# Optimization experiments

Hardware: AMD Instinct MI355X
Metric: run time of the kernel (lower is better)

The kernel has to match this reference:

```python
import jax, jax.numpy as jnp
import numpy as np

N_NODES = 50000
N_EDGES = 800000
D_IN = 64
D_OUT = 64


def setup_inputs() -> dict:
    key = jax.random.key(0)
    ks = jax.random.split(key, 7)
    features = jax.random.normal(ks[0], (N_NODES, D_IN), dtype=jnp.float32)
    # Linear(in,out,bias=False) weight: (out_features, in_features)
    W = jax.random.normal(ks[1], (D_OUT, D_IN), dtype=jnp.float32) / np.sqrt(D_IN)
    bias = jnp.zeros((D_OUT,), dtype=jnp.float32)
    skip_weight = jnp.ones((D_OUT,), dtype=jnp.float32)
    # sparse normalized adjacency as an edge list with scalar weights
    edge_src = jax.random.randint(ks[2], (N_EDGES,), 0, N_NODES, dtype=jnp.int32)
    edge_dst = jax.random.randint(ks[3], (N_EDGES,), 0, N_NODES, dtype=jnp.int32)
    edge_weight = jax.random.uniform(ks[4], (N_EDGES,), dtype=jnp.float32)
    return {
        "features": features,
        "W": W,
        "bias": bias,
        "skip_weight": skip_weight,
        "edge_weight": edge_weight,
        "edge_src": edge_src,
        "edge_dst": edge_dst,
    }


def reference(features, W, bias, skip_weight, edge_weight, edge_src, edge_dst):
    # Feature transform: x @ W^T  -> (n, out_features)
    h = jnp.einsum("nd,od->no", features, W)
    # Skip term: elementwise scale of transformed features
    skip = h * skip_weight
    # Sparse SpMM: aggregate weighted neighbor messages
    msgs = h[edge_src] * edge_weight[:, None]          # (E, out)
    agg = jax.ops.segment_sum(msgs, edge_dst, num_segments=N_NODES)  # (n, out)
    out = skip + agg + bias
    return jax.nn.selu(out)
```

## Files before the change

### kernel.cpp

```cpp
#include <hip/hip_runtime.h>
#include <math.h>

#define N_NODES 50000
#define N_EDGES 800000
#define D 64
#define NB2 782
#define BCAP2 2048
#define EPB 4096
#define NSCAT 196
#define GROWS 128
#define NGEMM ((N_NODES + GROWS - 1) / GROWS)

__device__ __forceinline__ float selu_f(float x) {
    const float scale = 1.0507009873554805f;
    const float alpha = 1.6732632423543772f;
    return x > 0.0f ? scale * x : scale * alpha * expm1f(x);
}

__device__ __forceinline__ unsigned int f2bf(float x) {
    unsigned int u = __float_as_uint(x);
    u += 0x7FFFu + ((u >> 16) & 1u);
    return u >> 16;
}

__device__ __forceinline__ float bf2f(unsigned int b) {
    return __uint_as_float(b << 16);
}

__global__ __launch_bounds__(1024) void fused_gemm_scatter(const float* __restrict__ feat,
                                                           const float* __restrict__ W,
                                                           const int* __restrict__ edst,
                                                           const int* __restrict__ esrc,
                                                           const float* __restrict__ ew,
                                                           unsigned short* __restrict__ hb,
                                                           int* __restrict__ gcursor,
                                                           int2* __restrict__ pay) {
    extern __shared__ char smem[];
    const int tid = threadIdx.x;

    if (blockIdx.x < NSCAT) {
        int* hist    = (int*)smem;
        int* lexcl   = hist + NB2;
        int* gbase   = lexcl + NB2;
        int* waveAgg = gbase + NB2;
        int2* stage  = (int2*)(waveAgg + 16);

        const int wid = tid >> 6;
        const int lane = tid & 63;
        const int e0 = blockIdx.x * EPB;
        const int cntb = min(EPB, N_EDGES - e0);

        for (int i = tid; i < NB2; i += 1024) hist[i] = 0;
        __syncthreads();

        int2 rec[4];
        int rb[4];
#pragma unroll
        for (int k = 0; k < 4; ++k) {
            const int idx = k * 1024 + tid;
            rb[k] = -1;
            if (idx < cntb) {
                const int e = e0 + idx;
                const int dst = edst[e];
                const int b = dst >> 6;
                rb[k] = b;
                rec[k] = make_int2((esrc[e] & 0xFFFF) | ((dst & 63) << 16) | (b << 22),
                                   __float_as_int(ew[e]));
                atomicAdd(&hist[b], 1);
            }
        }
        __syncthreads();

        const int v = (tid < NB2) ? hist[tid] : 0;
        int incl = v;
#pragma unroll
        for (int off = 1; off < 64; off <<= 1) {
            const int t = __shfl_up(incl, off);
            if (lane >= off) incl += t;
        }
        if (lane == 63) waveAgg[wid] = incl;
        __syncthreads();
        if (wid == 0) {
            const int wv = (lane < 16) ? waveAgg[lane] : 0;
            int wincl = wv;
#pragma unroll
            for (int off = 1; off < 16; off <<= 1) {
                const int t = __shfl_up(wincl, off);
                if (lane >= off) wincl += t;
            }
            if (lane < 16) waveAgg[lane] = wincl - wv;
        }
        __syncthreads();
        if (tid < NB2) {
            const int excl = incl - v + waveAgg[wid];
            lexcl[tid] = excl;
            hist[tid] = excl;
            gbase[tid] = (v > 0) ? atomicAdd(&gcursor[tid], v) : 0;
        }
        __syncthreads();

#pragma unroll
        for (int k = 0; k < 4; ++k) {
            if (rb[k] >= 0) {
                const int p = atomicAdd(&hist[rb[k]], 1);
                stage[p] = rec[k];
            }
        }
        __syncthreads();

        for (int i = tid; i < cntb; i += 1024) {
            const int2 r = stage[i];
            const int b = ((unsigned int)r.x) >> 22;
            const int g = gbase[b] + (i - lexcl[b]);
            if (g < BCAP2) pay[(size_t)b * BCAP2 + g] = r;
        }
    } else {
        float* Wt = (float*)smem;
        float* Sf = Wt + 64 * 68;
        const int base = (blockIdx.x - NSCAT) * GROWS;

        for (int i = tid; i < D * D; i += 1024) {
            int o = i >> 6, d = i & 63;
            Wt[d * 68 + o] = W[i];
        }
        for (int i = tid; i < GROWS * D; i += 1024) {
            int r = i >> 6, c = i & 63;
            int row = base + r;
            Sf[r * 68 + c] = (row < N_NODES) ? feat[(size_t)row * D + c] : 0.0f;
        }
        __syncthreads();

        const int r = tid >> 3;
        const int cg = tid & 7;
        const int row = base + r;
        if (row >= N_NODES) return;

        float4 a0 = {0, 0, 0, 0}, a1 = {0, 0, 0, 0};
        const float* WtC = Wt + cg * 8;
        const float* SfR = Sf + r * 68;
#pragma unroll 8
        for (int k = 0; k < D; ++k) {
            const float f = SfR[k];
            const float4 w0 = *(const float4*)(WtC + k * 68);
            const float4 w1 = *(const float4*)(WtC + k * 68 + 4);
            a0.x += f * w0.x; a0.y += f * w0.y; a0.z += f * w0.z; a0.w += f * w0.w;
            a1.x += f * w1.x; a1.y += f * w1.y; a1.z += f * w1.z; a1.w += f * w1.w;
        }

        uint4 p;
        p.x = f2bf(a0.x) | (f2bf(a0.y) << 16);
        p.y = f2bf(a0.z) | (f2bf(a0.w) << 16);
        p.z = f2bf(a1.x) | (f2bf(a1.y) << 16);
        p.w = f2bf(a1.z) | (f2bf(a1.w) << 16);
        *(uint4*)(hb + (size_t)row * D + cg * 8) = p;
    }
}

__global__ __launch_bounds__(512) void csr_sort(const int* __restrict__ gcursor,
                                                int2* __restrict__ pay,
                                                int2* __restrict__ nodeinfo) {
    __shared__ int2 stage[BCAP2];
    __shared__ int cntL[64], curL[64];

    const int b = blockIdx.x;
    const int tid = threadIdx.x;
    const int cnt = min(gcursor[b], BCAP2);
    int2* payb = pay + (size_t)b * BCAP2;

    if (tid < 64) cntL[tid] = 0;
    __syncthreads();

    for (int i = tid; i < cnt; i += 512) {
        const int2 r = payb[i];
        stage[i] = r;
        atomicAdd(&cntL[(r.x >> 16) & 63], 1);
    }
    __syncthreads();

    if (tid < 64) {
        const int v = cntL[tid];
        int incl = v;
#pragma unroll
        for (int off = 1; off < 64; off <<= 1) {
            const int t = __shfl_up(incl, off);
            if (tid >= off) incl += t;
        }
        const int excl = incl - v;
        curL[tid] = excl;
        const int node = (b << 6) + tid;
        if (node < N_NODES) nodeinfo[node] = make_int2(b * BCAP2 + excl, v);
    }
    __syncthreads();

    for (int i = tid; i < cnt; i += 512) {
        const int2 r = stage[i];
        const int p = atomicAdd(&curL[(r.x >> 16) & 63], 1);
        payb[p] = r;
    }
}

__global__ __launch_bounds__(256) void agg_epilogue_kernel(const unsigned short* __restrict__ hb,
                                                           const int2* __restrict__ nodeinfo,
                                                           const int2* __restrict__ pay,
                                                           const float* __restrict__ bias,
                                                           const float* __restrict__ skipw,
                                                           float* __restrict__ out) {
    const int gtid = blockIdx.x * 256 + threadIdx.x;
    const int n = gtid >> 6;
    const int lane = gtid & 63;
    if (n >= N_NODES) return;

    const int half = lane >> 5;
    const int sl = lane & 31;

    const int2 info = nodeinfo[n];
    const int beg = info.x;
    const int deg = info.y;

    float a0x = 0.f, a0y = 0.f, a1x = 0.f, a1y = 0.f;
    float a2x = 0.f, a2y = 0.f, a3x = 0.f, a3y = 0.f;

    for (int i = 0; i < deg; i += 64) {
        const int cnt = min(64, deg - i);
        int2 sw = make_int2(0, 0);
        if (lane < cnt) sw = pay[beg + i + lane];

        int j = 0;
        for (; j + 7 < cnt; j += 8) {
            const int s0 = __shfl(sw.x, j + 0 + half) & 0xFFFF;
            const int s1 = __shfl(sw.x, j + 2 + half) & 0xFFFF;
            const int s2 = __shfl(sw.x, j + 4 + half) & 0xFFFF;
            const int s3 = __shfl(sw.x, j + 6 + half) & 0xFFFF;
            const float w0 = __int_as_float(__shfl(sw.y, j + 0 + half));
            const float w1 = __int_as_float(__shfl(sw.y, j + 2 + half));
            const float w2 = __int_as_float(__shfl(sw.y, j + 4 + half));
            const float w3 = __int_as_float(__shfl(sw.y, j + 6 + half));
            const unsigned int g0 = *(const unsigned int*)(hb + ((size_t)s0 << 6) + sl * 2);
            const unsigned int g1 = *(const unsigned int*)(hb + ((size_t)s1 << 6) + sl * 2);
            const unsigned int g2 = *(const unsigned int*)(hb + ((size_t)s2 << 6) + sl * 2);
            const unsigned int g3 = *(const unsigned int*)(hb + ((size_t)s3 << 6) + sl * 2);
            a0x += bf2f(g0 & 0xFFFF) * w0;  a0y += bf2f(g0 >> 16) * w0;
            a1x += bf2f(g1 & 0xFFFF) * w1;  a1y += bf2f(g1 >> 16) * w1;
            a2x += bf2f(g2 & 0xFFFF) * w2;  a2y += bf2f(g2 >> 16) * w2;
            a3x += bf2f(g3 & 0xFFFF) * w3;  a3y += bf2f(g3 >> 16) * w3;
        }
        for (; j + 1 < cnt; j += 2) {
            const int s = __shfl(sw.x, j + half) & 0xFFFF;
            const float w = __int_as_float(__shfl(sw.y, j + half));
            const unsigned int g = *(const unsigned int*)(hb + ((size_t)s << 6) + sl * 2);
            a0x += bf2f(g & 0xFFFF) * w;  a0y += bf2f(g >> 16) * w;
        }
        if (j < cnt) {
            const int s = __shfl(sw.x, j) & 0xFFFF;
            const float w = __int_as_float(__shfl(sw.y, j));
            const unsigned int g = *(const unsigned int*)(hb + ((size_t)s << 6) + sl * 2);
            const float m = (half == 0) ? 1.0f : 0.0f;
            a1x += bf2f(g & 0xFFFF) * w * m;  a1y += bf2f(g >> 16) * w * m;
        }
    }

    float sx = (a0x + a1x) + (a2x + a3x);
    float sy = (a0y + a1y) + (a2y + a3y);
    sx += __shfl_xor(sx, 32);
    sy += __shfl_xor(sy, 32);

    const unsigned int hn = *(const unsigned int*)(hb + ((size_t)n << 6) + sl * 2);
    const float2 kv = ((const float2*)skipw)[sl];
    const float2 bv = ((const float2*)bias)[sl];
    if (half == 0) {
        float2 o;
        o.x = selu_f(bf2f(hn & 0xFFFF) * kv.x + bv.x + sx);
        o.y = selu_f(bf2f(hn >> 16) * kv.y + bv.y + sy);
        ((float2*)(out + ((size_t)n << 6)))[sl] = o;
    }
}

extern "C" void kernel_launch(void* const* d_in, const int* in_sizes, int n_in,
                              void* d_out, int out_size, void* d_ws, size_t ws_size,
                              hipStream_t stream) {
    const float* feat  = (const float*)d_in[0];
    const float* W     = (const float*)d_in[1];
    const float* bias  = (const float*)d_in[2];
    const float* skipw = (const float*)d_in[3];
    const float* ew    = (const float*)d_in[4];
    const int*   esrc  = (const int*)d_in[5];
    const int*   edst  = (const int*)d_in[6];
    float* out = (float*)d_out;

    int2*           pay      = (int2*)d_ws;
    unsigned short* hb       = (unsigned short*)(pay + (size_t)NB2 * BCAP2);
    int2*           nodeinfo = (int2*)(hb + (size_t)N_NODES * D);
    int*            gcursor  = (int*)(nodeinfo + N_NODES);

    hipMemsetAsync(gcursor, 0, (size_t)NB2 * sizeof(int), stream);

    const size_t smem = (size_t)(64 * 68 + GROWS * 68) * sizeof(float);
    fused_gemm_scatter<<<NSCAT + NGEMM, 1024, smem, stream>>>(feat, W, edst, esrc, ew,
                                                              hb, gcursor, pay);

    csr_sort<<<NB2, 512, 0, stream>>>(gcursor, pay, nodeinfo);

    agg_epilogue_kernel<<<(N_NODES * 64 + 255) / 256, 256, 0, stream>>>(
        hb, nodeinfo, pay, bias, skipw, out);
}
```

Baseline: 131.0 us.

## Replace global atomic bucket cursors with per-block fixed slabs and count prefix

Each scatter block now writes its per-bucket counts to a count matrix and places its records in a private fixed-capacity slot (32 entries) inside each bucket's slab, instead of reserving space through global atomicAdd cursors. The CSR sort kernel computes a prefix sum over the per-block counts to compact the slab into a staging buffer, then sorts as before. This removes the global atomics and the memset launch, and makes record placement deterministic. In exchange the payload workspace grows several-fold, the sort kernel scans sparse slots, and any bucket receiving more than 32 edges from one block silently drops records.

```diff
diff --git a/kernel.cpp b/kernel.cpp
--- a/kernel.cpp
+++ b/kernel.cpp
@@ -8,6 +8,8 @@
 #define BCAP2 2048
 #define EPB 4096
 #define NSCAT 196
+#define CAPB 32
+#define SLAB (NSCAT * CAPB)
 #define GROWS 128
 #define NGEMM ((N_NODES + GROWS - 1) / GROWS)
 
@@ -33,7 +35,7 @@
                                                            const int* __restrict__ esrc,
                                                            const float* __restrict__ ew,
                                                            unsigned short* __restrict__ hb,
-                                                           int* __restrict__ gcursor,
+                                                           int* __restrict__ cnts,
                                                            int2* __restrict__ pay) {
     extern __shared__ char smem[];
     const int tid = threadIdx.x;
@@ -41,8 +43,7 @@
     if (blockIdx.x < NSCAT) {
         int* hist    = (int*)smem;
         int* lexcl   = hist + NB2;
-        int* gbase   = lexcl + NB2;
-        int* waveAgg = gbase + NB2;
+        int* waveAgg = lexcl + NB2;
         int2* stage  = (int2*)(waveAgg + 16);
 
         const int wid = tid >> 6;
@@ -95,7 +96,7 @@
             const int excl = incl - v + waveAgg[wid];
             lexcl[tid] = excl;
             hist[tid] = excl;
-            gbase[tid] = (v > 0) ? atomicAdd(&gcursor[tid], v) : 0;
+            cnts[blockIdx.x * NB2 + tid] = v;
         }
         __syncthreads();
 
@@ -111,8 +112,8 @@
         for (int i = tid; i < cntb; i += 1024) {
             const int2 r = stage[i];
             const int b = ((unsigned int)r.x) >> 22;
-            const int g = gbase[b] + (i - lexcl[b]);
-            if (g < BCAP2) pay[(size_t)b * BCAP2 + g] = r;
+            const int off = i - lexcl[b];
+            if (off < CAPB) pay[(size_t)b * SLAB + blockIdx.x * CAPB + off] = r;
         }
     } else {
         float* Wt = (float*)smem;
@@ -156,43 +157,82 @@
     }
 }
 
-__global__ __launch_bounds__(512) void csr_sort(const int* __restrict__ gcursor,
+__global__ __launch_bounds__(512) void csr_sort(const int* __restrict__ cnts,
                                                 int2* __restrict__ pay,
                                                 int2* __restrict__ nodeinfo) {
     __shared__ int2 stage[BCAP2];
+    __shared__ int cntS[NSCAT];
+    __shared__ int runoff[NSCAT];
+    __shared__ int waveAgg[8];
     __shared__ int cntL[64], curL[64];
 
     const int b = blockIdx.x;
     const int tid = threadIdx.x;
-    const int cnt = min(gcursor[b], BCAP2);
-    int2* payb = pay + (size_t)b * BCAP2;
+    const int wid = tid >> 6;
+    const int lane = tid & 63;
+    int2* payb = pay + (size_t)b * SLAB;
 
     if (tid < 64) cntL[tid] = 0;
-    __syncthreads();
-
-    for (int i = tid; i < cnt; i += 512) {
-        const int2 r = payb[i];
-        stage[i] = r;
-        atomicAdd(&cntL[(r.x >> 16) & 63], 1);
-    }
-    __syncthreads();
+
+    const int c = (tid < NSCAT) ? cnts[tid * NB2 + b] : 0;
+
+    int incl = c;
+#pragma unroll
+    for (int off = 1; off < 64; off <<= 1) {
+        const int t = __shfl_up(incl, off);
+        if (lane >= off) incl += t;
+    }
+    if (lane == 63) waveAgg[wid] = incl;
+    __syncthreads();
+    if (wid == 0) {
+        const int wv = (lane < 8) ? waveAgg[lane] : 0;
+        int wincl = wv;
+#pragma unroll
+        for (int off = 1; off < 8; off <<= 1) {
+            const int t = __shfl_up(wincl, off);
+            if (lane >= off) wincl += t;
+        }
+        if (lane < 8) waveAgg[lane] = wincl - wv;
+    }
+    __syncthreads();
+    if (tid < NSCAT) {
+        cntS[tid] = c;
+        runoff[tid] = incl - c + waveAgg[wid];
+    }
+    __syncthreads();
+
+    for (int i = tid; i < NSCAT * CAPB; i += 512) {
+        const int blk = i >> 5;
+        const int pos = i & (CAPB - 1);
+        if (pos < cntS[blk]) {
+            const int p = runoff[blk] + pos;
+            if (p < BCAP2) {
+                const int2 r = payb[i];
+                stage[p] = r;
+                atomicAdd(&cntL[(r.x >> 16) & 63], 1);
+            }
+        }
+    }
+    __syncthreads();
+
+    const int total = min(runoff[NSCAT - 1] + cntS[NSCAT - 1], BCAP2);
 
     if (tid < 64) {
         const int v = cntL[tid];
-        int incl = v;
+        int inc2 = v;
 #pragma unroll
         for (int off = 1; off < 64; off <<= 1) {
-            const int t = __shfl_up(incl, off);
-            if (tid >= off) incl += t;
-        }
-        const int excl = incl - v;
+            const int t = __shfl_up(inc2, off);
+            if (tid >= off) inc2 += t;
+        }
+        const int excl = inc2 - v;
         curL[tid] = excl;
         const int node = (b << 6) + tid;
-        if (node < N_NODES) nodeinfo[node] = make_int2(b * BCAP2 + excl, v);
-    }
-    __syncthreads();
-
-    for (int i = tid; i < cnt; i += 512) {
+        if (node < N_NODES) nodeinfo[node] = make_int2(b * SLAB + excl, v);
+    }
+    __syncthreads();
+
+    for (int i = tid; i < total; i += 512) {
         const int2 r = stage[i];
         const int p = atomicAdd(&curL[(r.x >> 16) & 63], 1);
         payb[p] = r;
@@ -288,17 +328,15 @@
     float* out = (float*)d_out;
 
     int2*           pay      = (int2*)d_ws;
-    unsigned short* hb       = (unsigned short*)(pay + (size_t)NB2 * BCAP2);
+    unsigned short* hb       = (unsigned short*)(pay + (size_t)NB2 * SLAB);
     int2*           nodeinfo = (int2*)(hb + (size_t)N_NODES * D);
-    int*            gcursor  = (int*)(nodeinfo + N_NODES);
-
-    hipMemsetAsync(gcursor, 0, (size_t)NB2 * sizeof(int), stream);
+    int*            cnts     = (int*)(nodeinfo + N_NODES);
 
     const size_t smem = (size_t)(64 * 68 + GROWS * 68) * sizeof(float);
     fused_gemm_scatter<<<NSCAT + NGEMM, 1024, smem, stream>>>(feat, W, edst, esrc, ew,
-                                                              hb, gcursor, pay);
-
-    csr_sort<<<NB2, 512, 0, stream>>>(gcursor, pay, nodeinfo);
+                                                              hb, cnts, pay);
+
+    csr_sort<<<NB2, 512, 0, stream>>>(cnts, pay, nodeinfo);
 
     agg_epilogue_kernel<<<(N_NODES * 64 + 255) / 256, 256, 0, stream>>>(
         hb, nodeinfo, pay, bias, skipw, out);
```

After: 131.4 us. No clear change (+0.4%).
